# Performance work log

Hardware: AMD Instinct MI355X
Metric: run time of the kernel (lower is better)

The kernel has to match this reference:

```python
import jax, jax.numpy as jnp
import numpy as np

HEADS = 4
HEAD_DIM = 24
PH, PW = 2, 2  # proposal grid -> M = PH*PW = 4 prototype centers
EPS = 1e-12


def setup_inputs() -> dict:
    key = jax.random.key(0)
    ks = jax.random.split(key, 6)
    B, Cin, H, W = 16, 128, 112, 112
    Cout = 128
    D = HEADS * HEAD_DIM  # 96
    x = jax.random.normal(ks[0], (B, Cin, H, W), jnp.float32)
    # 1x1 conv weights stored as [out, in] (kernel dims squeezed)
    f_w = jax.random.normal(ks[1], (D, Cin), jnp.float32) / np.float32(np.sqrt(Cin))
    f_b = jnp.zeros((D,), jnp.float32)
    v_w = jax.random.normal(ks[2], (D, Cin), jnp.float32) / np.float32(np.sqrt(Cin))
    v_b = jnp.zeros((D,), jnp.float32)
    proj_w = jax.random.normal(ks[3], (Cout, D), jnp.float32) / np.float32(np.sqrt(D))
    proj_b = jnp.zeros((Cout,), jnp.float32)
    sim_alpha = jnp.ones((1,), jnp.float32)
    sim_beta = jnp.zeros((1,), jnp.float32)
    # OrthogonalPriorGenerator: Gram-Schmidt orthonormalized random rows
    rng = np.random.default_rng(0)
    W0 = rng.standard_normal((HEAD_DIM, PH * PW)).astype(np.float32) * np.sqrt(2.0 / HEAD_DIM).astype(np.float32)
    q, _ = np.linalg.qr(W0)  # orthonormal columns
    centers = jnp.asarray(q.T, jnp.float32)  # [M, head_dim], orthonormal rows
    return {"x": x, "f_w": f_w, "f_b": f_b, "v_w": v_w, "v_b": v_b,
            "proj_w": proj_w, "proj_b": proj_b,
            "sim_alpha": sim_alpha, "sim_beta": sim_beta, "centers": centers}


def reference(x, f_w, f_b, v_w, v_b, proj_w, proj_b, sim_alpha, sim_beta, centers):
    B, Cin, H, W = x.shape
    M = PH * PW
    c = HEAD_DIM
    bh = B * HEADS
    n = H * W
    # 1x1 convs
    f = jnp.einsum('oi,bihw->bohw', f_w, x) + f_b[None, :, None, None]
    v = jnp.einsum('oi,bihw->bohw', v_w, x) + v_b[None, :, None, None]
    # split heads into batch: b (e c) h w -> (b e) c h w
    f = f.reshape(bh, c, n)                      # [(be), c, n]
    v4 = v.reshape(bh, c, H, W)                  # [(be), c, h, w]
    # adaptive avg pool to (PH, PW) -> value centers [(be), M, c]
    vc = v4.reshape(bh, c, PH, H // PH, PW, W // PW).mean(axis=(3, 5))
    value_centers = vc.reshape(bh, c, M).transpose(0, 2, 1)
    # cosine similarity of orthonormal centers vs tokens
    cn = centers / jnp.maximum(jnp.linalg.norm(centers, axis=-1, keepdims=True), EPS)
    xn = f.transpose(0, 2, 1)                    # [(be), n, c]
    xn = xn / jnp.maximum(jnp.linalg.norm(xn, axis=-1, keepdims=True), EPS)
    sim = jax.nn.sigmoid(sim_beta + sim_alpha * jnp.einsum('mc,bnc->bmn', cn, xn))
    # hard top-1 assignment mask over centers
    idx = jnp.argmax(sim, axis=1)                # [(be), n]
    mask = jax.nn.one_hot(idx, M, axis=1, dtype=sim.dtype)  # [(be), M, n]
    sim = sim * mask
    # dispatch: weighted aggregation into centers
    value2 = v4.reshape(bh, c, n).transpose(0, 2, 1)          # [(be), n, c]
    agg = (jnp.einsum('bmn,bnc->bmc', sim, value2) + value_centers)
    agg = agg / (sim.sum(axis=-1, keepdims=True) + 1.0)
    # combine: redistribute center features back to tokens
    out = jnp.einsum('bmn,bmc->bnc', sim, agg)                # [(be), n, c]
    out = out.transpose(0, 2, 1).reshape(B, HEADS * c, H, W)  # merge heads
    out = jnp.einsum('oi,bihw->bohw', proj_w, out) + proj_b[None, :, None, None]
    assignment_map = idx[0].reshape(H, W)
    return out, assignment_map
```

## Files before the change

### kernel.cpp

```cpp
#include <hip/hip_runtime.h>
#include <hip/hip_bf16.h>

namespace {

constexpr int kCin   = 128;
constexpr int kHW    = 12544;
constexpr int kW     = 112;
constexpr int kGrps  = 49;
constexpr int kTiles = 196;
constexpr size_t kOut1Off = (size_t)16 * 128 * kHW;

typedef __attribute__((ext_vector_type(8))) short short8;
typedef __attribute__((ext_vector_type(4))) float f32x4;

__device__ __forceinline__ float bf2f(unsigned short u) {
  union { unsigned int i; float f; } v;
  v.i = ((unsigned int)u) << 16;
  return v.f;
}

__device__ __forceinline__ unsigned short f2bf(float f) {
  union { float f; unsigned int i; } v;
  v.f = f;
  unsigned int x = v.i;
  x += 0x7fffu + ((x >> 16) & 1u);
  return (unsigned short)(x >> 16);
}

template <bool BF>
__device__ __forceinline__ float ld1(const void* p, size_t i) {
  if constexpr (BF) return bf2f(((const unsigned short*)p)[i]);
  else              return ((const float*)p)[i];
}
template <bool BF>
__device__ __forceinline__ void ld4(const void* p, size_t i, float o[4]) {
  if constexpr (BF) {
    const ushort4 u = *reinterpret_cast<const ushort4*>((const unsigned short*)p + i);
    o[0] = bf2f(u.x); o[1] = bf2f(u.y); o[2] = bf2f(u.z); o[3] = bf2f(u.w);
  } else {
    const float4 u = *reinterpret_cast<const float4*>((const float*)p + i);
    o[0] = u.x; o[1] = u.y; o[2] = u.z; o[3] = u.w;
  }
}
template <bool BF>
__device__ __forceinline__ void st1(void* p, size_t i, float v) {
  if constexpr (BF) ((unsigned short*)p)[i] = f2bf(v);
  else              ((float*)p)[i] = v;
}
template <bool BF>
__device__ __forceinline__ void st4(void* p, size_t i, const float v[4]) {
  if constexpr (BF) {
    ushort4 u;
    u.x = f2bf(v[0]); u.y = f2bf(v[1]); u.z = f2bf(v[2]); u.w = f2bf(v[3]);
    *reinterpret_cast<ushort4*>((unsigned short*)p + i) = u;
  } else {
    float4 u;
    u.x = v[0]; u.y = v[1]; u.z = v[2]; u.w = v[3];
    *reinterpret_cast<float4*>((float*)p + i) = u;
  }
}

__global__ void detect_dtype(const unsigned short* __restrict__ fw, int* __restrict__ flag) {
  __shared__ int cnt_s;
  if (threadIdx.x == 0) cnt_s = 0;
  __syncthreads();
  int c = 0;
  for (int i = threadIdx.x; i < 4096; i += 256) {
    const float v = bf2f(fw[i]);
    if (fabsf(v) > 4.0f) ++c;
  }
  atomicAdd(&cnt_s, c);
  __syncthreads();
  if (threadIdx.x == 0) flag[0] = (cnt_s > 100) ? 0 : 1;
}

struct alignas(16) SMain {
  union {
    unsigned short xt[64][136];
    float fh[96 * 65];
  } u;
  float cn[4][24];
  float s[4][64];
  unsigned char idx[4][64];
  unsigned char q[64];
};

template <bool BF>
__device__ __forceinline__ void main_body(
    SMain& sm,
    const void* __restrict__ x,  const void* __restrict__ f_w, const void* __restrict__ f_b,
    const void* __restrict__ v_w, const void* __restrict__ v_b,
    const void* __restrict__ sim_alpha, const void* __restrict__ sim_beta,
    const void* __restrict__ centers,
    void* __restrict__ out0,
    float* __restrict__ aggsum, float* __restrict__ vpool, float* __restrict__ cnt)
{
  const int tid  = threadIdx.x;
  const int b    = blockIdx.x / kTiles;
  const int tile = blockIdx.x % kTiles;
  const int hw0  = tile * 64;

  if (tid < 4) {
    float cv[24];
    float n2 = 0.f;
#pragma unroll
    for (int c = 0; c < 24; ++c) { cv[c] = ld1<BF>(centers, tid * 24 + c); n2 += cv[c] * cv[c]; }
    const float inv = 1.f / fmaxf(sqrtf(n2), 1e-12f);
#pragma unroll
    for (int c = 0; c < 24; ++c) sm.cn[tid][c] = cv[c] * inv;
  }
  const float alpha = ld1<BF>(sim_alpha, 0);
  const float beta  = ld1<BF>(sim_beta, 0);

  const int e   = tid >> 6;
  const int tok = tid & 63;

  const int lane = tid & 63;
  const int wv   = tid >> 6;
  const int qq   = lane >> 4;
  const int tt   = lane & 15;
  f32x4 accB[3][4];
  float biasB[3][4];
  int   wrb = 0;
  bool  isfB = true;

  const int ty = tid >> 4;
  const int tx = tid & 15;
  const bool is_f = (ty < 8);
  float acc[12][4];
  float bias[12];

  if constexpr (BF) {
#pragma unroll
    for (int s5 = 0; s5 < 8; ++s5) {
      const int id2 = tid + s5 * 256;
      const int ch  = id2 >> 4;
      const int tg  = id2 & 15;
      const ushort4 u4 = *reinterpret_cast<const ushort4*>(
          (const unsigned short*)x + ((size_t)b * kCin + ch) * kHW + hw0 + tg * 4);
      sm.u.xt[tg * 4 + 0][ch] = u4.x;
      sm.u.xt[tg * 4 + 1][ch] = u4.y;
      sm.u.xt[tg * 4 + 2][ch] = u4.z;
      sm.u.xt[tg * 4 + 3][ch] = u4.w;
    }
    const int wbase = wv * 48;
    isfB = (wv < 2);
    const unsigned short* wselB = (const unsigned short*)(isfB ? f_w : v_w);
    const void* bselB = isfB ? f_b : v_b;
    wrb = isfB ? wbase : wbase - 96;
#pragma unroll
    for (int rt = 0; rt < 3; ++rt)
#pragma unroll
      for (int rg = 0; rg < 4; ++rg)
        biasB[rt][rg] = ld1<true>(bselB, (size_t)(wrb + rt * 16 + qq * 4 + rg));
    __syncthreads();

    const f32x4 z4 = {0.f, 0.f, 0.f, 0.f};
#pragma unroll
    for (int rt = 0; rt < 3; ++rt)
#pragma unroll
      for (int ct = 0; ct < 4; ++ct) accB[rt][ct] = z4;

#pragma unroll
    for (int rt = 0; rt < 3; ++rt) {
      short8 afr[4];
#pragma unroll
      for (int k = 0; k < 4; ++k)
        afr[k] = *reinterpret_cast<const short8*>(
            wselB + (size_t)(wrb + rt * 16 + tt) * 128 + k * 32 + qq * 8);
#pragma unroll
      for (int ct = 0; ct < 4; ++ct) {
#pragma unroll
        for (int k = 0; k < 4; ++k) {
          const short8 bfr = *reinterpret_cast<const short8*>(
              &sm.u.xt[ct * 16 + tt][k * 32 + qq * 8]);
          accB[rt][ct] = __builtin_amdgcn_mfma_f32_16x16x32_bf16(afr[k], bfr, accB[rt][ct], 0, 0, 0);
        }
      }
    }
    __syncthreads();

    if (isfB) {
#pragma unroll
      for (int rt = 0; rt < 3; ++rt)
#pragma unroll
        for (int ct = 0; ct < 4; ++ct)
#pragma unroll
          for (int rg = 0; rg < 4; ++rg)
            sm.u.fh[(wrb + rt * 16 + qq * 4 + rg) * 65 + ct * 16 + tt] =
                accB[rt][ct][rg] + biasB[rt][rg];
    }
  } else {
    const void*  wsel  = is_f ? f_w : v_w;
    const void*  bsel  = is_f ? f_b : v_b;
    const size_t wrow0 = (size_t)(is_f ? ty * 12 : ty * 12 - 96);
#pragma unroll
    for (int r = 0; r < 12; ++r) bias[r] = ld1<false>(bsel, wrow0 + r);
#pragma unroll
    for (int r = 0; r < 12; ++r)
#pragma unroll
      for (int j = 0; j < 4; ++j) acc[r][j] = 0.f;

    const size_t xbase = ((size_t)b * kCin) * kHW + hw0 + tx * 4;
    for (int i = 0; i < 128; i += 4) {
      float xv[4][4];
#pragma unroll
      for (int ci = 0; ci < 4; ++ci) ld4<false>(x, xbase + (size_t)(i + ci) * kHW, xv[ci]);
      float wvr[6][4];
#pragma unroll
      for (int r = 0; r < 6; ++r) ld4<false>(wsel, (wrow0 + r) * 128 + i, wvr[r]);
#pragma unroll
      for (int r = 0; r < 6; ++r)
#pragma unroll
        for (int ci = 0; ci < 4; ++ci)
#pragma unroll
          for (int j = 0; j < 4; ++j)
            acc[r][j] = fmaf(wvr[r][ci], xv[ci][j], acc[r][j]);
#pragma unroll
      for (int r = 0; r < 6; ++r) ld4<false>(wsel, (wrow0 + 6 + r) * 128 + i, wvr[r]);
#pragma unroll
      for (int r = 0; r < 6; ++r)
#pragma unroll
        for (int ci = 0; ci < 4; ++ci)
#pragma unroll
          for (int j = 0; j < 4; ++j)
            acc[6 + r][j] = fmaf(wvr[r][ci], xv[ci][j], acc[6 + r][j]);
    }
    if (is_f) {
#pragma unroll
      for (int r = 0; r < 12; ++r)
#pragma unroll
        for (int j = 0; j < 4; ++j)
          sm.u.fh[(ty * 12 + r) * 65 + tx * 4 + j] = acc[r][j] + bias[r];
    }
  }
  __syncthreads();

  {
    float dm[4] = {0.f, 0.f, 0.f, 0.f};
    float n2 = 0.f;
#pragma unroll
    for (int c = 0; c < 24; ++c) {
      const float fc = sm.u.fh[(e * 24 + c) * 65 + tok];
      n2 += fc * fc;
      dm[0] += fc * sm.cn[0][c];
      dm[1] += fc * sm.cn[1][c];
      dm[2] += fc * sm.cn[2][c];
      dm[3] += fc * sm.cn[3][c];
    }
    const float inv = 1.f / fmaxf(sqrtf(n2), 1e-12f);
    float s[4];
#pragma unroll
    for (int m = 0; m < 4; ++m) {
      const float z = beta + alpha * dm[m] * inv;
      s[m] = 1.f / (1.f + __expf(-z));
    }
    float best = -1.f;
    int bi = 0;
#pragma unroll
    for (int m = 0; m < 4; ++m)
      if (s[m] > best) { best = s[m]; bi = m; }

    const int hw = hw0 + tok;
    st1<BF>(out0, ((size_t)(b * 128 + e)) * kHW + hw, best);
    st1<BF>(out0, ((size_t)(b * 128 + 4 + e)) * kHW + hw, (float)bi);
    sm.s[e][tok]   = best;
    sm.idx[e][tok] = (unsigned char)bi;
    if (e == 0) {
      const int h = hw / kW;
      const int w = hw - h * kW;
      sm.q[tok] = (unsigned char)((h >= 56 ? 2 : 0) + (w >= 56 ? 1 : 0));
    }
  }
  __syncthreads();

  if constexpr (BF) {
    if (!isfB) {
#pragma unroll
      for (int rt = 0; rt < 3; ++rt)
#pragma unroll
        for (int ct = 0; ct < 4; ++ct)
#pragma unroll
          for (int rg = 0; rg < 4; ++rg)
            sm.u.fh[(wrb + rt * 16 + qq * 4 + rg) * 65 + ct * 16 + tt] =
                accB[rt][ct][rg] + biasB[rt][rg];
    }
  } else {
    if (!is_f) {
#pragma unroll
      for (int r = 0; r < 12; ++r)
#pragma unroll
        for (int j = 0; j < 4; ++j)
          sm.u.fh[((ty - 8) * 12 + r) * 65 + tx * 4 + j] = acc[r][j] + bias[r];
    }
  }
  __syncthreads();

  float agg_m[4]  = {0.f, 0.f, 0.f, 0.f};
  float pool_q[4] = {0.f, 0.f, 0.f, 0.f};
  float cacc = 0.f;
  if (tid < 192) {
    const int half = tid / 96;
    const int c    = tid - half * 96;
    const int eh   = c / 24;
    const int row0 = c * 65;
    const int t20  = half * 32;
    for (int k = 0; k < 32; ++k) {
      const int t2 = t20 + k;
      const float v = sm.u.fh[row0 + t2];
      const float s = sm.s[eh][t2];
      const int  mi = sm.idx[eh][t2];
      const int  q  = sm.q[t2];
      const float sv = s * v;
      agg_m[0]  += (mi == 0) ? sv : 0.f;
      agg_m[1]  += (mi == 1) ? sv : 0.f;
      agg_m[2]  += (mi == 2) ? sv : 0.f;
      agg_m[3]  += (mi == 3) ? sv : 0.f;
      pool_q[0] += (q == 0) ? v : 0.f;
      pool_q[1] += (q == 1) ? v : 0.f;
      pool_q[2] += (q == 2) ? v : 0.f;
      pool_q[3] += (q == 3) ? v : 0.f;
    }
    const int cc  = c % 24;
    const int bh  = b * 4 + eh;
#pragma unroll
    for (int m = 0; m < 4; ++m) {
      atomicAdd(&aggsum[(bh * 4 + m) * 24 + cc], agg_m[m]);
      atomicAdd(&vpool[(bh * 4 + m) * 24 + cc], pool_q[m]);
    }
  } else if (tid < 224) {
    const int p  = tid - 192;
    const int em = p >> 1;
    const int ce = em >> 2, cm = em & 3;
    const int t20 = (p & 1) * 32;
    for (int k = 0; k < 32; ++k) {
      const int t2 = t20 + k;
      cacc += (sm.idx[ce][t2] == cm) ? sm.s[ce][t2] : 0.f;
    }
    atomicAdd(&cnt[b * 16 + em], cacc);
  }
}

__global__ __launch_bounds__(256, 2) void cluster_main(
    const int* __restrict__ flag,
    const void* x, const void* f_w, const void* f_b, const void* v_w, const void* v_b,
    const void* sim_alpha, const void* sim_beta, const void* centers,
    void* out0, float* aggsum, float* vpool, float* cnt)
{
  __shared__ SMain sm;
  if (*flag)
    main_body<true>(sm, x, f_w, f_b, v_w, v_b, sim_alpha, sim_beta, centers, out0, aggsum, vpool, cnt);
  else
    main_body<false>(sm, x, f_w, f_b, v_w, v_b, sim_alpha, sim_beta, centers, out0, aggsum, vpool, cnt);
}

struct SOut {
  float af[384];
  float p[2048];
  float pb[128];
};

template <bool BF>
__device__ __forceinline__ void out_body(
    SOut& so, const void* __restrict__ proj_w, const void* __restrict__ proj_b,
    const float* __restrict__ aggsum, const float* __restrict__ vpool,
    const float* __restrict__ cnt, void* __restrict__ out0)
{
  const int tid = threadIdx.x;
  const int b   = blockIdx.x / kGrps;
  const int grp = blockIdx.x % kGrps;

  for (int k = tid; k < 384; k += 256) {
    const int em = k / 24;
    so.af[k] = (aggsum[b * 384 + k] + vpool[b * 384 + k] * (1.f / 3136.f)) / (cnt[b * 16 + em] + 1.f);
  }
  if (tid < 128) so.pb[tid] = ld1<BF>(proj_b, tid);
  __syncthreads();
#pragma unroll
  for (int i = 0; i < 8; ++i) {
    const int g  = i * 256 + tid;
    const int o  = g >> 4;
    const int em = g & 15;
    const int e  = em >> 2;
    float a = 0.f;
#pragma unroll
    for (int c = 0; c < 24; ++c)
      a = fmaf(ld1<BF>(proj_w, (size_t)o * 96 + e * 24 + c), so.af[em * 24 + c], a);
    so.p[g] = a;
  }
  __syncthreads();

  const int tgi = tid & 31;
  const int cg  = tid >> 5;
  const int hw  = grp * 256 + tgi * 8;
  const size_t base = ((size_t)(b * 128)) * kHW + hw;

  float sv[4][8];
  int   mi[4][8];
  float ivh[8];
#pragma unroll
  for (int e2 = 0; e2 < 4; ++e2) {
    ld4<BF>(out0, base + (size_t)e2 * kHW,     &sv[e2][0]);
    ld4<BF>(out0, base + (size_t)e2 * kHW + 4, &sv[e2][4]);
    float iv[8];
    ld4<BF>(out0, base + (size_t)(4 + e2) * kHW,     &iv[0]);
    ld4<BF>(out0, base + (size_t)(4 + e2) * kHW + 4, &iv[4]);
#pragma unroll
    for (int j = 0; j < 8; ++j) {
      mi[e2][j] = (int)(iv[j] + 0.5f);
      if (e2 == 0) ivh[j] = iv[j];
    }
  }
  __syncthreads();

  if (b == 0 && cg == 0) {
    st4<BF>(out0, kOut1Off + hw,     &ivh[0]);
    st4<BF>(out0, kOut1Off + hw + 4, &ivh[4]);
  }

#pragma unroll
  for (int oi = 0; oi < 16; ++oi) {
    const int o = cg * 16 + oi;
    const float* pr  = &so.p[o * 16];
    const float  pbv = so.pb[o];
    float ov[8];
#pragma unroll
    for (int j = 0; j < 8; ++j) {
      float a = pbv;
      a = fmaf(sv[0][j], pr[ 0 + mi[0][j]], a);
      a = fmaf(sv[1][j], pr[ 4 + mi[1][j]], a);
      a = fmaf(sv[2][j], pr[ 8 + mi[2][j]], a);
      a = fmaf(sv[3][j], pr[12 + mi[3][j]], a);
      ov[j] = a;
    }
    st4<BF>(out0, base + (size_t)o * kHW,     &ov[0]);
    st4<BF>(out0, base + (size_t)o * kHW + 4, &ov[4]);
  }
}

__global__ __launch_bounds__(256) void cluster_out(
    const int* __restrict__ flag,
    const void* proj_w, const void* proj_b,
    const float* __restrict__ aggsum, const float* __restrict__ vpool,
    const float* __restrict__ cnt, void* out0)
{
  __shared__ SOut so;
  if (*flag) out_body<true>(so, proj_w, proj_b, aggsum, vpool, cnt, out0);
  else       out_body<false>(so, proj_w, proj_b, aggsum, vpool, cnt, out0);
}

}

extern "C" void kernel_launch(void* const* d_in, const int* in_sizes, int n_in,
                              void* d_out, int out_size, void* d_ws, size_t ws_size,
                              hipStream_t stream) {
  const void* x         = d_in[0];
  const void* f_w       = d_in[1];
  const void* f_b       = d_in[2];
  const void* v_w       = d_in[3];
  const void* v_b       = d_in[4];
  const void* proj_w    = d_in[5];
  const void* proj_b    = d_in[6];
  const void* sim_alpha = d_in[7];
  const void* sim_beta  = d_in[8];
  const void* centers   = d_in[9];

  int*   flag   = (int*)d_ws;
  float* fws    = (float*)((char*)d_ws + 16);
  float* aggsum = fws;
  float* vpool  = fws + 6144;
  float* cnt    = fws + 12288;

  hipMemsetAsync(d_ws, 0, 16 + 12544 * sizeof(float), stream);

  detect_dtype<<<dim3(1), dim3(256), 0, stream>>>((const unsigned short*)f_w, flag);
  cluster_main<<<dim3(16 * kTiles), dim3(256), 0, stream>>>(
      flag, x, f_w, f_b, v_w, v_b, sim_alpha, sim_beta, centers,
      d_out, aggsum, vpool, cnt);
  cluster_out<<<dim3(16 * kGrps), dim3(256), 0, stream>>>(
      flag, proj_w, proj_b, aggsum, vpool, cnt, d_out);
}
```

Before: 486.4 us.

## Replace global atomics with per-block partials and a separate reduction kernel

Each main block now stages its per-center aggregation, pooled values and counts in shared memory, combines the two halves, and writes a 784-float partial record to the workspace instead of issuing many global atomicAdds. A new small kernel sums the 196 tile partials per batch and writes aggsum, vpool and cnt, which also removes the workspace memset. This targets contention from atomics on a small set of addresses. The cost is an extra kernel launch, extra workspace traffic, and a reduction kernel with only 49 blocks doing strided serial sums.

```diff
diff --git a/kernel.cpp b/kernel.cpp
--- a/kernel.cpp
+++ b/kernel.cpp
@@ -92,8 +92,7 @@
     const void* __restrict__ v_w, const void* __restrict__ v_b,
     const void* __restrict__ sim_alpha, const void* __restrict__ sim_beta,
     const void* __restrict__ centers,
-    void* __restrict__ out0,
-    float* __restrict__ aggsum, float* __restrict__ vpool, float* __restrict__ cnt)
+    void* __restrict__ out0, float* __restrict__ partial)
 {
   const int tid  = threadIdx.x;
   const int b    = blockIdx.x / kTiles;
@@ -321,13 +320,6 @@
       pool_q[2] += (q == 2) ? v : 0.f;
       pool_q[3] += (q == 3) ? v : 0.f;
     }
-    const int cc  = c % 24;
-    const int bh  = b * 4 + eh;
-#pragma unroll
-    for (int m = 0; m < 4; ++m) {
-      atomicAdd(&aggsum[(bh * 4 + m) * 24 + cc], agg_m[m]);
-      atomicAdd(&vpool[(bh * 4 + m) * 24 + cc], pool_q[m]);
-    }
   } else if (tid < 224) {
     const int p  = tid - 192;
     const int em = p >> 1;
@@ -337,7 +329,33 @@
       const int t2 = t20 + k;
       cacc += (sm.idx[ce][t2] == cm) ? sm.s[ce][t2] : 0.f;
     }
-    atomicAdd(&cnt[b * 16 + em], cacc);
+  }
+  __syncthreads();
+
+  float* red = sm.u.fh;
+  if (tid < 192) {
+    const int half = tid / 96;
+    const int c    = tid - half * 96;
+    float* r = &red[(half * 96 + c) * 8];
+    r[0] = agg_m[0]; r[1] = agg_m[1]; r[2] = agg_m[2]; r[3] = agg_m[3];
+    r[4] = pool_q[0]; r[5] = pool_q[1]; r[6] = pool_q[2]; r[7] = pool_q[3];
+  } else if (tid < 224) {
+    red[1536 + (tid - 192)] = cacc;
+  }
+  __syncthreads();
+
+  float* pt = &partial[(size_t)blockIdx.x * 784];
+  if (tid < 96) {
+    const int c = tid;
+#pragma unroll
+    for (int m = 0; m < 4; ++m)
+      pt[m * 96 + c] = red[c * 8 + m] + red[(96 + c) * 8 + m];
+#pragma unroll
+    for (int q2 = 0; q2 < 4; ++q2)
+      pt[384 + q2 * 96 + c] = red[c * 8 + 4 + q2] + red[(96 + c) * 8 + 4 + q2];
+  } else if (tid < 112) {
+    const int em = tid - 96;
+    pt[768 + em] = red[1536 + 2 * em] + red[1536 + 2 * em + 1];
   }
 }
 
@@ -345,13 +363,37 @@
     const int* __restrict__ flag,
     const void* x, const void* f_w, const void* f_b, const void* v_w, const void* v_b,
     const void* sim_alpha, const void* sim_beta, const void* centers,
-    void* out0, float* aggsum, float* vpool, float* cnt)
+    void* out0, float* __restrict__ partial)
 {
   __shared__ SMain sm;
   if (*flag)
-    main_body<true>(sm, x, f_w, f_b, v_w, v_b, sim_alpha, sim_beta, centers, out0, aggsum, vpool, cnt);
+    main_body<true>(sm, x, f_w, f_b, v_w, v_b, sim_alpha, sim_beta, centers, out0, partial);
   else
-    main_body<false>(sm, x, f_w, f_b, v_w, v_b, sim_alpha, sim_beta, centers, out0, aggsum, vpool, cnt);
+    main_body<false>(sm, x, f_w, f_b, v_w, v_b, sim_alpha, sim_beta, centers, out0, partial);
+}
+
+__global__ void cluster_red(const float* __restrict__ partial,
+                            float* __restrict__ aggsum, float* __restrict__ vpool,
+                            float* __restrict__ cnt) {
+  const int g = blockIdx.x * 256 + threadIdx.x;
+  if (g >= 16 * 784) return;
+  const int b = g / 784;
+  const int v = g - b * 784;
+  const float* base = partial + (size_t)b * kTiles * 784 + v;
+  float s = 0.f;
+#pragma unroll 4
+  for (int t = 0; t < kTiles; ++t) s += base[(size_t)t * 784];
+  if (v < 384) {
+    const int m = v / 96, c = v - m * 96;
+    const int eh = c / 24, cc = c - eh * 24;
+    aggsum[b * 384 + (eh * 4 + m) * 24 + cc] = s;
+  } else if (v < 768) {
+    const int q = (v - 384) / 96, c = (v - 384) - q * 96;
+    const int eh = c / 24, cc = c - eh * 24;
+    vpool[b * 384 + (eh * 4 + q) * 24 + cc] = s;
+  } else {
+    cnt[b * 16 + (v - 768)] = s;
+  }
 }
 
 struct SOut {
@@ -465,18 +507,18 @@
   const void* sim_beta  = d_in[8];
   const void* centers   = d_in[9];
 
-  int*   flag   = (int*)d_ws;
-  float* fws    = (float*)((char*)d_ws + 16);
-  float* aggsum = fws;
-  float* vpool  = fws + 6144;
-  float* cnt    = fws + 12288;
-
-  hipMemsetAsync(d_ws, 0, 16 + 12544 * sizeof(float), stream);
+  int*   flag    = (int*)d_ws;
+  float* fws     = (float*)((char*)d_ws + 16);
+  float* aggsum  = fws;
+  float* vpool   = fws + 6144;
+  float* cnt     = fws + 12288;
+  float* partial = fws + 12544;
 
   detect_dtype<<<dim3(1), dim3(256), 0, stream>>>((const unsigned short*)f_w, flag);
   cluster_main<<<dim3(16 * kTiles), dim3(256), 0, stream>>>(
       flag, x, f_w, f_b, v_w, v_b, sim_alpha, sim_beta, centers,
-      d_out, aggsum, vpool, cnt);
+      d_out, partial);
+  cluster_red<<<dim3(49), dim3(256), 0, stream>>>(partial, aggsum, vpool, cnt);
   cluster_out<<<dim3(16 * kGrps), dim3(256), 0, stream>>>(
       flag, proj_w, proj_b, aggsum, vpool, cnt, d_out);
 }
```

After: 440.9 us. 1.1x faster.
